# Performance work log

Measured on AMD Instinct MI355X. Metric: run time of the kernel, lower is better.

The kernel has to match this reference:

```python
import jax, jax.numpy as jnp
import numpy as np

B, N, C = 4, 1024, 768          # batch, tokens, embed_dim
D, H, HD, FF = 12, 12, 64, 3072  # depth, heads, head_dim, mlp hidden
LN_EPS = 1e-5


def setup_inputs() -> dict:
    key = jax.random.key(0)
    ks = jax.random.split(key, 12)
    w = lambda i, shape: jax.random.normal(ks[i], shape, jnp.float32) * 0.02
    return {
        "x": jax.random.normal(ks[0], (B, N, C), jnp.float32),
        "pos_x": jax.random.normal(ks[1], (B, N, C), jnp.float32),
        # stacked per-layer params (leading dim D)
        "qkv_w": w(2, (D, 3 * C, C)), "qkv_b": w(3, (D, 3 * C)),
        "proj_w": w(4, (D, C, C)),    "proj_b": w(5, (D, C)),
        "fc1_w": w(6, (D, FF, C)),    "fc1_b": w(7, (D, FF)),
        "fc2_w": w(8, (D, C, FF)),    "fc2_b": w(9, (D, C)),
        "ln1_g": jnp.ones((D, C), jnp.float32), "ln1_b": jnp.zeros((D, C), jnp.float32),
        "ln2_g": jnp.ones((D, C), jnp.float32), "ln2_b": jnp.zeros((D, C), jnp.float32),
        "normf_g": jnp.ones((C,), jnp.float32), "normf_b": jnp.zeros((C,), jnp.float32),
    }


def _ln(x, g, b):
    mu = jnp.mean(x, axis=-1, keepdims=True)
    var = jnp.mean((x - mu) ** 2, axis=-1, keepdims=True)
    return (x - mu) * jax.lax.rsqrt(var + LN_EPS) * g + b


def reference(x, pos_x, qkv_w, qkv_b, proj_w, proj_b, fc1_w, fc1_b, fc2_w, fc2_b,
              ln1_g, ln1_b, ln2_g, ln2_b, normf_g, normf_b):
    scale = 1.0 / jnp.sqrt(jnp.float32(HD))
    x = x + pos_x  # pos added once (add_pos_at_every_layer=False)

    def block(xc, p):
        qw, qb, pw, pb, f1w, f1b, f2w, f2b, g1, b1, g2, b2 = p
        h = _ln(xc, g1, b1)
        qkv = jnp.einsum('bnc,oc->bno', h, qw) + qb            # [B,N,3C]
        qkv = qkv.reshape(B, N, 3, H, HD).transpose(2, 0, 3, 1, 4)
        q, k, v = qkv[0], qkv[1], qkv[2]                       # [B,H,N,HD]
        attn = jax.nn.softmax(jnp.einsum('bhnd,bhmd->bhnm', q, k) * scale, axis=-1)
        o = jnp.einsum('bhnm,bhmd->bhnd', attn, v)
        o = o.transpose(0, 2, 1, 3).reshape(B, N, C)
        xc = xc + (jnp.einsum('bnc,oc->bno', o, pw) + pb)      # residual + proj
        h2 = _ln(xc, g2, b2)
        hid = jax.nn.gelu(jnp.einsum('bnc,fc->bnf', h2, f1w) + f1b, approximate=False)
        ffn = jnp.einsum('bnf,of->bno', hid, f2w) + f2b
        xc = xc + ffn
        return xc, None

    xs = (qkv_w, qkv_b, proj_w, proj_b, fc1_w, fc1_b, fc2_w, fc2_b,
          ln1_g, ln1_b, ln2_g, ln2_b)
    x, _ = jax.lax.scan(block, x, xs)
    return _ln(x, normf_g, normf_b)  # postnorm
```

## Files before the change

kernel.cpp:

```cpp
#include <hip/hip_runtime.h>
#include <hip/hip_bf16.h>
#include <math.h>

typedef __bf16 bf16;
typedef __bf16 bf16x8 __attribute__((ext_vector_type(8)));
typedef __bf16 bf16x4 __attribute__((ext_vector_type(4)));
typedef float  f32x4  __attribute__((ext_vector_type(4)));

#define B_  4
#define N_  1024
#define C_  768
#define H_  12
#define HD_ 64
#define FF_ 3072
#define T_  (B_*N_)
#define D_  12

__device__ __forceinline__ void gld_lds16(const void* g, void* l) {
    __builtin_amdgcn_global_load_lds(
        (const __attribute__((address_space(1))) void*)g,
        (__attribute__((address_space(3))) void*)l, 16, 0, 0);
}

template<typename WT, int MODE>
__global__ __launch_bounds__(256) void gemm_bt(
    const bf16* __restrict__ A, const WT* __restrict__ Bt,
    const float* __restrict__ bias, bf16* __restrict__ out,
    float* __restrict__ resid, int M, int N, int Kfull, int Ks)
{
    __shared__ __align__(16) bf16 lA[128*64];
    __shared__ __align__(16) WT   lB[128*64];
    const int tid  = threadIdx.x;
    const int lane = tid & 63, wave = tid >> 6;
    const int lo = lane & 15, hi = lane >> 4;
    const int wm = wave & 1, wn = wave >> 1;
    const int row0 = blockIdx.x * 128, col0 = blockIdx.y * 128;
    const int k0base = blockIdx.z * Ks;

    f32x4 acc[4][4];
#pragma unroll
    for (int i = 0; i < 4; i++)
#pragma unroll
        for (int j = 0; j < 4; j++) acc[i][j] = (f32x4){0.f, 0.f, 0.f, 0.f};

    for (int k0 = k0base; k0 < k0base + Ks; k0 += 64) {
#pragma unroll
        for (int r = 0; r < 4; ++r) {
            const int cb    = r * 256 + wave * 64;
            const int chunk = cb + lane;
            const int rw = chunk >> 3, kc = chunk & 7;
            const int kcs = kc ^ (rw & 7);
            gld_lds16(A + (size_t)(row0 + rw) * Kfull + k0 + kcs * 8, lA + cb * 8);
        }
        if constexpr (sizeof(WT) == 2) {
#pragma unroll
            for (int r = 0; r < 4; ++r) {
                const int cb    = r * 256 + wave * 64;
                const int chunk = cb + lane;
                const int rw = chunk >> 3, kc = chunk & 7;
                const int kcs = kc ^ (rw & 7);
                gld_lds16(Bt + (size_t)(col0 + rw) * Kfull + k0 + kcs * 8,
                          (bf16*)lB + cb * 8);
            }
        } else {
#pragma unroll
            for (int r = 0; r < 8; ++r) {
                const int cb    = r * 256 + wave * 64;
                const int chunk = cb + lane;
                const int rw = chunk >> 4, kc = chunk & 15;
                const int kcs = kc ^ ((rw & 7) << 1);
                gld_lds16(Bt + (size_t)(col0 + rw) * Kfull + k0 + kcs * 4,
                          (float*)lB + cb * 4);
            }
        }
        __syncthreads();
#pragma unroll 1
        for (int s = 0; s < 2; ++s) {
            bf16x8 af[4], bfr[4];
#pragma unroll
            for (int i = 0; i < 4; i++) {
                const int rowA = wm * 64 + i * 16 + lo;
                const int ca = (s * 4 + hi) ^ (lo & 7);
                af[i] = *(const bf16x8*)(lA + rowA * 64 + ca * 8);
            }
#pragma unroll
            for (int i = 0; i < 4; i++) {
                const int rowB = wn * 64 + i * 16 + lo;
                if constexpr (sizeof(WT) == 2) {
                    const int cb = (s * 4 + hi) ^ (lo & 7);
                    bfr[i] = *(const bf16x8*)((const bf16*)lB + rowB * 64 + cb * 8);
                } else {
                    const float* base = (const float*)lB + rowB * 64;
                    const int c0 = (s * 8 + hi * 2) ^ ((lo & 7) << 1);
                    const f32x4 u0 = *(const f32x4*)(base + c0 * 4);
                    const f32x4 u1 = *(const f32x4*)(base + (c0 + 1) * 4);
                    bf16x8 f;
#pragma unroll
                    for (int e = 0; e < 4; e++) { f[e] = (bf16)u0[e]; f[4+e] = (bf16)u1[e]; }
                    bfr[i] = f;
                }
            }
#pragma unroll
            for (int mi = 0; mi < 4; mi++)
#pragma unroll
                for (int ni = 0; ni < 4; ni++)
                    acc[mi][ni] = __builtin_amdgcn_mfma_f32_16x16x32_bf16(
                        af[mi], bfr[ni], acc[mi][ni], 0, 0, 0);
        }
        __syncthreads();
    }

    const float bscale = (blockIdx.z == 0) ? 1.0f : 0.0f;
#pragma unroll
    for (int mi = 0; mi < 4; mi++) {
#pragma unroll
        for (int ni = 0; ni < 4; ni++) {
            const int gcol = col0 + wn * 64 + ni * 16 + lo;
            const float bv = bias[gcol] * bscale;
#pragma unroll
            for (int r = 0; r < 4; r++) {
                const int grow = row0 + wm * 64 + mi * 16 + hi * 4 + r;
                float v = acc[mi][ni][r] + bv;
                if (MODE == 1) v = 0.5f * v * (1.0f + erff(v * 0.70710678118f));
                if (MODE == 2) {
                    atomicAdd(&resid[(size_t)grow * N + gcol], v);
                } else {
                    out[(size_t)grow * N + gcol] = (bf16)v;
                }
            }
        }
    }
}

__global__ __launch_bounds__(256) void cvt_k(
    const float* __restrict__ src, bf16* __restrict__ dst)
{
    const int i = (blockIdx.x * 256 + threadIdx.x) * 8;
    const f32x4 a = *(const f32x4*)(src + i);
    const f32x4 b = *(const f32x4*)(src + i + 4);
    bf16x8 o;
#pragma unroll
    for (int e = 0; e < 4; e++) { o[e] = (bf16)a[e]; o[4 + e] = (bf16)b[e]; }
    *(bf16x8*)(dst + i) = o;
}

template<typename OutT>
__global__ __launch_bounds__(256) void ln_k(
    const float* __restrict__ x, const float* __restrict__ g,
    const float* __restrict__ b, OutT* __restrict__ out)
{
    const int wave = threadIdx.x >> 6, lane = threadIdx.x & 63;
    const int t = blockIdx.x * 4 + wave;
    const float* row = x + (size_t)t * C_;
    f32x4 v[3];
    float s = 0.f, ss = 0.f;
#pragma unroll
    for (int j = 0; j < 3; j++) {
        v[j] = *(const f32x4*)(row + (j * 64 + lane) * 4);
#pragma unroll
        for (int e = 0; e < 4; e++) { s += v[j][e]; ss += v[j][e] * v[j][e]; }
    }
#pragma unroll
    for (int off = 32; off > 0; off >>= 1) {
        s  += __shfl_xor(s, off);
        ss += __shfl_xor(ss, off);
    }
    const float mu  = s * (1.f / 768.f);
    const float var = ss * (1.f / 768.f) - mu * mu;
    const float rs  = rsqrtf(var + 1e-5f);
    OutT* orow = out + (size_t)t * C_;
#pragma unroll
    for (int j = 0; j < 3; j++) {
        const f32x4 gv = *(const f32x4*)(g + (j * 64 + lane) * 4);
        const f32x4 bv = *(const f32x4*)(b + (j * 64 + lane) * 4);
#pragma unroll
        for (int e = 0; e < 4; e++)
            orow[(j * 64 + lane) * 4 + e] = (OutT)((v[j][e] - mu) * rs * gv[e] + bv[e]);
    }
}

__global__ __launch_bounds__(256) void addpos_k(
    const float* __restrict__ x, const float* __restrict__ p, float* __restrict__ o)
{
    const int i = (blockIdx.x * 256 + threadIdx.x) * 4;
    const f32x4 xv = *(const f32x4*)(x + i);
    const f32x4 pv = *(const f32x4*)(p + i);
    f32x4 ov;
#pragma unroll
    for (int e = 0; e < 4; e++) ov[e] = xv[e] + pv[e];
    *(f32x4*)(o + i) = ov;
}

#define SKD_ 72
#define SVK_ 136
#define SPK_ 136
__global__ __launch_bounds__(256) void attn_k(
    const bf16* __restrict__ qkv, bf16* __restrict__ out)
{
    const int qt = blockIdx.x;
    const int bh = blockIdx.y;
    const int b = bh / H_, h = bh % H_;
    const int lane = threadIdx.x & 63, wave = threadIdx.x >> 6;
    const int lo = lane & 15, hi = lane >> 4;

    __shared__ __align__(16) bf16 lK[128 * SKD_];
    __shared__ __align__(16) bf16 lV[64 * SVK_];
    __shared__ __align__(16) bf16 lP[4][16 * SPK_];

    const size_t tokbase = (size_t)b * N_;

    const bf16* qptr = qkv + (tokbase + qt * 64 + wave * 16 + lo) * (3 * C_) + h * HD_;
    bf16x8 qf0 = *(const bf16x8*)(qptr + hi * 8);
    bf16x8 qf1 = *(const bf16x8*)(qptr + 32 + hi * 8);
#pragma unroll
    for (int e = 0; e < 8; e++) {
        qf0[e] = (bf16)((float)qf0[e] * 0.125f);
        qf1[e] = (bf16)((float)qf1[e] * 0.125f);
    }

    float m_r[4], l_r[4];
    f32x4 oacc[4];
#pragma unroll
    for (int r = 0; r < 4; r++) { m_r[r] = -1e30f; l_r[r] = 0.f; }
#pragma unroll
    for (int di = 0; di < 4; di++) oacc[di] = (f32x4){0.f, 0.f, 0.f, 0.f};

    for (int kt = 0; kt < 8; ++kt) {
        const int kb0 = kt * 128;
#pragma unroll
        for (int r = 0; r < 4; ++r) {
            const int chunk = r * 256 + threadIdx.x;
            const int key = chunk >> 3, dc = chunk & 7;
            const bf16* kp = qkv + (tokbase + kb0 + key) * (3 * C_) + C_ + h * HD_ + dc * 8;
            *(bf16x8*)(lK + key * SKD_ + dc * 8) = *(const bf16x8*)kp;
        }
#pragma unroll
        for (int r = 0; r < 4; ++r) {
            const int chunk = r * 256 + threadIdx.x;
            const int d = chunk & 63, kg = chunk >> 6;
            const bf16* vp = qkv + (tokbase + kb0 + kg * 8) * (3 * C_)
                           + 2 * C_ + h * HD_ + d;
            bf16x8 tv;
#pragma unroll
            for (int i = 0; i < 8; i++) tv[i] = vp[(size_t)i * (3 * C_)];
            *(bf16x8*)(lV + d * SVK_ + kg * 8) = tv;
        }
        __syncthreads();

        f32x4 sacc[8];
#pragma unroll
        for (int kb = 0; kb < 8; kb++) {
            const bf16x8 b0 = *(const bf16x8*)(lK + (kb * 16 + lo) * SKD_ + hi * 8);
            const bf16x8 b1 = *(const bf16x8*)(lK + (kb * 16 + lo) * SKD_ + 32 + hi * 8);
            f32x4 a = (f32x4){0.f, 0.f, 0.f, 0.f};
            a = __builtin_amdgcn_mfma_f32_16x16x32_bf16(qf0, b0, a, 0, 0, 0);
            a = __builtin_amdgcn_mfma_f32_16x16x32_bf16(qf1, b1, a, 0, 0, 0);
            sacc[kb] = a;
        }

        float tm[4], mn[4], alpha[4], ts[4];
#pragma unroll
        for (int r = 0; r < 4; r++) {
            float a0 = fmaxf(fmaxf(sacc[0][r], sacc[1][r]),
                             fmaxf(sacc[2][r], sacc[3][r]));
            float a1 = fmaxf(fmaxf(sacc[4][r], sacc[5][r]),
                             fmaxf(sacc[6][r], sacc[7][r]));
            tm[r] = fmaxf(a0, a1);
#pragma unroll
            for (int off = 1; off < 16; off <<= 1)
                tm[r] = fmaxf(tm[r], __shfl_xor(tm[r], off));
            mn[r] = fmaxf(m_r[r], tm[r]);
            alpha[r] = __expf(m_r[r] - mn[r]);
            ts[r] = 0.f;
        }
#pragma unroll
        for (int kb = 0; kb < 8; kb++)
#pragma unroll
            for (int r = 0; r < 4; r++) {
                const float p = __expf(sacc[kb][r] - mn[r]);
                lP[wave][(hi * 4 + r) * SPK_ + kb * 16 + lo] = (bf16)p;
                ts[r] += p;
            }
#pragma unroll
        for (int r = 0; r < 4; r++) {
#pragma unroll
            for (int off = 1; off < 16; off <<= 1)
                ts[r] += __shfl_xor(ts[r], off);
            l_r[r] = l_r[r] * alpha[r] + ts[r];
            m_r[r] = mn[r];
        }
#pragma unroll
        for (int di = 0; di < 4; di++)
#pragma unroll
            for (int r = 0; r < 4; r++) oacc[di][r] *= alpha[r];

        bf16x8 pa[4];
#pragma unroll
        for (int s = 0; s < 4; s++)
            pa[s] = *(const bf16x8*)(&lP[wave][lo * SPK_ + s * 32 + hi * 8]);
#pragma unroll
        for (int di = 0; di < 4; di++) {
#pragma unroll
            for (int s = 0; s < 4; s++) {
                const bf16x8 v = *(const bf16x8*)(lV + (di * 16 + lo) * SVK_ + s * 32 + hi * 8);
                oacc[di] = __builtin_amdgcn_mfma_f32_16x16x32_bf16(pa[s], v, oacc[di], 0, 0, 0);
            }
        }
        __syncthreads();
    }

#pragma unroll
    for (int di = 0; di < 4; di++)
#pragma unroll
        for (int r = 0; r < 4; r++) {
            const size_t tok = tokbase + qt * 64 + wave * 16 + hi * 4 + r;
            out[tok * C_ + h * HD_ + di * 16 + lo] = (bf16)(oacc[di][r] / l_r[r]);
        }
}

extern "C" void kernel_launch(void* const* d_in, const int* in_sizes, int n_in,
                              void* d_out, int out_size, void* d_ws, size_t ws_size,
                              hipStream_t stream)
{
    const float* x      = (const float*)d_in[0];
    const float* pos_x  = (const float*)d_in[1];
    const float* qkv_w  = (const float*)d_in[2];
    const float* qkv_b  = (const float*)d_in[3];
    const float* proj_w = (const float*)d_in[4];
    const float* proj_b = (const float*)d_in[5];
    const float* fc1_w  = (const float*)d_in[6];
    const float* fc1_b  = (const float*)d_in[7];
    const float* fc2_w  = (const float*)d_in[8];
    const float* fc2_b  = (const float*)d_in[9];
    const float* ln1_g  = (const float*)d_in[10];
    const float* ln1_b  = (const float*)d_in[11];
    const float* ln2_g  = (const float*)d_in[12];
    const float* ln2_b  = (const float*)d_in[13];
    const float* nf_g   = (const float*)d_in[14];
    const float* nf_b   = (const float*)d_in[15];

    char* ws = (char*)d_ws;
    float* xres  = (float*)(ws);
    bf16* hbuf   = (bf16*)(ws + 12582912);
    bf16* qkvbuf = (bf16*)(ws + 18874368);
    bf16* attno  = (bf16*)(ws + 37748736);
    bf16* hid    = (bf16*)(ws + 44040192);
    bf16* wq     = (bf16*)(ws + 69206016);
    bf16* wp     = (bf16*)(ws + 111673344);
    bf16* w1     = (bf16*)(ws + 125829120);
    bf16* w2     = (bf16*)(ws + 182452224);
    const bool usebf16 = ws_size >= (size_t)239075328;

    addpos_k<<<T_ * C_ / 4 / 256, 256, 0, stream>>>(x, pos_x, xres);

    if (usebf16) {
        cvt_k<<<D_ * 3 * C_ * C_ / 2048, 256, 0, stream>>>(qkv_w, wq);
        cvt_k<<<D_ * C_ * C_ / 2048, 256, 0, stream>>>(proj_w, wp);
        cvt_k<<<D_ * FF_ * C_ / 2048, 256, 0, stream>>>(fc1_w, w1);
        cvt_k<<<D_ * C_ * FF_ / 2048, 256, 0, stream>>>(fc2_w, w2);
    }

    for (int L = 0; L < D_; ++L) {
        ln_k<bf16><<<T_ / 4, 256, 0, stream>>>(xres, ln1_g + L * C_, ln1_b + L * C_, hbuf);
        if (usebf16) {
            gemm_bt<bf16,0><<<dim3(T_/128, (3*C_)/128, 1), 256, 0, stream>>>(
                hbuf, wq + (size_t)L * 3 * C_ * C_, qkv_b + (size_t)L * 3 * C_,
                qkvbuf, nullptr, T_, 3 * C_, C_, C_);
        } else {
            gemm_bt<float,0><<<dim3(T_/128, (3*C_)/128, 1), 256, 0, stream>>>(
                hbuf, qkv_w + (size_t)L * 3 * C_ * C_, qkv_b + (size_t)L * 3 * C_,
                qkvbuf, nullptr, T_, 3 * C_, C_, C_);
        }
        attn_k<<<dim3(N_ / 64, B_ * H_), 256, 0, stream>>>(qkvbuf, attno);
        if (usebf16) {
            gemm_bt<bf16,2><<<dim3(T_/128, C_/128, 2), 256, 0, stream>>>(
                attno, wp + (size_t)L * C_ * C_, proj_b + (size_t)L * C_,
                nullptr, xres, T_, C_, C_, C_ / 2);
        } else {
            gemm_bt<float,2><<<dim3(T_/128, C_/128, 2), 256, 0, stream>>>(
                attno, proj_w + (size_t)L * C_ * C_, proj_b + (size_t)L * C_,
                nullptr, xres, T_, C_, C_, C_ / 2);
        }
        ln_k<bf16><<<T_ / 4, 256, 0, stream>>>(xres, ln2_g + L * C_, ln2_b + L * C_, hbuf);
        if (usebf16) {
            gemm_bt<bf16,1><<<dim3(T_/128, FF_/128, 1), 256, 0, stream>>>(
                hbuf, w1 + (size_t)L * FF_ * C_, fc1_b + (size_t)L * FF_,
                hid, nullptr, T_, FF_, C_, C_);
            gemm_bt<bf16,2><<<dim3(T_/128, C_/128, 2), 256, 0, stream>>>(
                hid, w2 + (size_t)L * C_ * FF_, fc2_b + (size_t)L * C_,
                nullptr, xres, T_, C_, FF_, FF_ / 2);
        } else {
            gemm_bt<float,1><<<dim3(T_/128, FF_/128, 1), 256, 0, stream>>>(
                hbuf, fc1_w + (size_t)L * FF_ * C_, fc1_b + (size_t)L * FF_,
                hid, nullptr, T_, FF_, C_, C_);
            gemm_bt<float,2><<<dim3(T_/128, C_/128, 2), 256, 0, stream>>>(
                hid, fc2_w + (size_t)L * C_ * FF_, fc2_b + (size_t)L * C_,
                nullptr, xres, T_, C_, FF_, FF_ / 2);
        }
    }
    ln_k<float><<<T_ / 4, 256, 0, stream>>>(xres, nf_g, nf_b, (float*)d_out);
}
```

Before: 2.647 ms.

## Remap GEMM and attention blocks across XCDs and defer softmax rescaling

```diff
diff --git a/kernel.cpp b/kernel.cpp
--- a/kernel.cpp
+++ b/kernel.cpp
@@ -34,8 +34,16 @@
     const int lane = tid & 63, wave = tid >> 6;
     const int lo = lane & 15, hi = lane >> 4;
     const int wm = wave & 1, wn = wave >> 1;
-    const int row0 = blockIdx.x * 128, col0 = blockIdx.y * 128;
-    const int k0base = blockIdx.z * Ks;
+
+    const int nblk = gridDim.x;
+    const int id2  = (blockIdx.x & 7) * (nblk >> 3) + (blockIdx.x >> 3);
+    const int gx = M >> 7, gy = N >> 7;
+    const int bx  = id2 % gx;
+    const int byz = id2 / gx;
+    const int by  = byz % gy;
+    const int bz  = byz / gy;
+    const int row0 = bx * 128, col0 = by * 128;
+    const int k0base = bz * Ks;
 
     f32x4 acc[4][4];
 #pragma unroll
@@ -110,7 +118,7 @@
         __syncthreads();
     }
 
-    const float bscale = (blockIdx.z == 0) ? 1.0f : 0.0f;
+    const float bscale = (bz == 0) ? 1.0f : 0.0f;
 #pragma unroll
     for (int mi = 0; mi < 4; mi++) {
 #pragma unroll
@@ -197,8 +205,9 @@
 __global__ __launch_bounds__(256) void attn_k(
     const bf16* __restrict__ qkv, bf16* __restrict__ out)
 {
-    const int qt = blockIdx.x;
-    const int bh = blockIdx.y;
+    const int id2 = (blockIdx.x & 7) * 96 + (blockIdx.x >> 3);
+    const int qt = id2 & 15;
+    const int bh = id2 >> 4;
     const int b = bh / H_, h = bh % H_;
     const int lane = threadIdx.x & 63, wave = threadIdx.x >> 6;
     const int lo = lane & 15, hi = lane >> 4;
@@ -258,20 +267,31 @@
             sacc[kb] = a;
         }
 
-        float tm[4], mn[4], alpha[4], ts[4];
+        float pm[4], mn[4], ts[4];
 #pragma unroll
         for (int r = 0; r < 4; r++) {
             float a0 = fmaxf(fmaxf(sacc[0][r], sacc[1][r]),
                              fmaxf(sacc[2][r], sacc[3][r]));
             float a1 = fmaxf(fmaxf(sacc[4][r], sacc[5][r]),
                              fmaxf(sacc[6][r], sacc[7][r]));
-            tm[r] = fmaxf(a0, a1);
-#pragma unroll
-            for (int off = 1; off < 16; off <<= 1)
-                tm[r] = fmaxf(tm[r], __shfl_xor(tm[r], off));
-            mn[r] = fmaxf(m_r[r], tm[r]);
-            alpha[r] = __expf(m_r[r] - mn[r]);
+            pm[r] = fmaxf(a0, a1);
             ts[r] = 0.f;
+        }
+        const int okd = (pm[0] <= m_r[0] + 8.f) && (pm[1] <= m_r[1] + 8.f)
+                     && (pm[2] <= m_r[2] + 8.f) && (pm[3] <= m_r[3] + 8.f);
+        const bool defer = __all(okd);
+        if (defer) {
+#pragma unroll
+            for (int r = 0; r < 4; r++) mn[r] = m_r[r];
+        } else {
+#pragma unroll
+            for (int r = 0; r < 4; r++) {
+                float tm = pm[r];
+#pragma unroll
+                for (int off = 1; off < 16; off <<= 1)
+                    tm = fmaxf(tm, __shfl_xor(tm, off));
+                mn[r] = fmaxf(m_r[r], tm);
+            }
         }
 #pragma unroll
         for (int kb = 0; kb < 8; kb++)
@@ -282,17 +302,26 @@
                 ts[r] += p;
             }
 #pragma unroll
-        for (int r = 0; r < 4; r++) {
+        for (int r = 0; r < 4; r++)
 #pragma unroll
             for (int off = 1; off < 16; off <<= 1)
                 ts[r] += __shfl_xor(ts[r], off);
-            l_r[r] = l_r[r] * alpha[r] + ts[r];
-            m_r[r] = mn[r];
-        }
-#pragma unroll
-        for (int di = 0; di < 4; di++)
-#pragma unroll
-            for (int r = 0; r < 4; r++) oacc[di][r] *= alpha[r];
+        if (defer) {
+#pragma unroll
+            for (int r = 0; r < 4; r++) l_r[r] += ts[r];
+        } else {
+            float alpha[4];
+#pragma unroll
+            for (int r = 0; r < 4; r++) {
+                alpha[r] = __expf(m_r[r] - mn[r]);
+                l_r[r] = l_r[r] * alpha[r] + ts[r];
+                m_r[r] = mn[r];
+            }
+#pragma unroll
+            for (int di = 0; di < 4; di++)
+#pragma unroll
+                for (int r = 0; r < 4; r++) oacc[di][r] *= alpha[r];
+        }
 
         bf16x8 pa[4];
 #pragma unroll
@@ -309,12 +338,15 @@
         __syncthreads();
     }
 
+    float il[4];
+#pragma unroll
+    for (int r = 0; r < 4; r++) il[r] = 1.0f / l_r[r];
 #pragma unroll
     for (int di = 0; di < 4; di++)
 #pragma unroll
         for (int r = 0; r < 4; r++) {
             const size_t tok = tokbase + qt * 64 + wave * 16 + hi * 4 + r;
-            out[tok * C_ + h * HD_ + di * 16 + lo] = (bf16)(oacc[di][r] / l_r[r]);
+            out[tok * C_ + h * HD_ + di * 16 + lo] = (bf16)(oacc[di][r] * il[r]);
         }
 }
 
@@ -360,40 +392,45 @@
         cvt_k<<<D_ * C_ * FF_ / 2048, 256, 0, stream>>>(fc2_w, w2);
     }
 
+    const int g_qkv  = (T_/128) * ((3*C_)/128);
+    const int g_proj = (T_/128) * (C_/128) * 2;
+    const int g_fc1  = (T_/128) * (FF_/128);
+    const int g_fc2  = (T_/128) * (C_/128) * 2;
+
     for (int L = 0; L < D_; ++L) {
         ln_k<bf16><<<T_ / 4, 256, 0, stream>>>(xres, ln1_g + L * C_, ln1_b + L * C_, hbuf);
         if (usebf16) {
-            gemm_bt<bf16,0><<<dim3(T_/128, (3*C_)/128, 1), 256, 0, stream>>>(
+            gemm_bt<bf16,0><<<g_qkv, 256, 0, stream>>>(
                 hbuf, wq + (size_t)L * 3 * C_ * C_, qkv_b + (size_t)L * 3 * C_,
                 qkvbuf, nullptr, T_, 3 * C_, C_, C_);
         } else {
-            gemm_bt<float,0><<<dim3(T_/128, (3*C_)/128, 1), 256, 0, stream>>>(
+            gemm_bt<float,0><<<g_qkv, 256, 0, stream>>>(
                 hbuf, qkv_w + (size_t)L * 3 * C_ * C_, qkv_b + (size_t)L * 3 * C_,
                 qkvbuf, nullptr, T_, 3 * C_, C_, C_);
         }
-        attn_k<<<dim3(N_ / 64, B_ * H_), 256, 0, stream>>>(qkvbuf, attno);
+        attn_k<<<N_ / 64 * B_ * H_, 256, 0, stream>>>(qkvbuf, attno);
         if (usebf16) {
-            gemm_bt<bf16,2><<<dim3(T_/128, C_/128, 2), 256, 0, stream>>>(
+            gemm_bt<bf16,2><<<g_proj, 256, 0, stream>>>(
                 attno, wp + (size_t)L * C_ * C_, proj_b + (size_t)L * C_,
                 nullptr, xres, T_, C_, C_, C_ / 2);
         } else {
-            gemm_bt<float,2><<<dim3(T_/128, C_/128, 2), 256, 0, stream>>>(
+            gemm_bt<float,2><<<g_proj, 256, 0, stream>>>(
                 attno, proj_w + (size_t)L * C_ * C_, proj_b + (size_t)L * C_,
                 nullptr, xres, T_, C_, C_, C_ / 2);
         }
         ln_k<bf16><<<T_ / 4, 256, 0, stream>>>(xres, ln2_g + L * C_, ln2_b + L * C_, hbuf);
         if (usebf16) {
-            gemm_bt<bf16,1><<<dim3(T_/128, FF_/128, 1), 256, 0, stream>>>(
+            gemm_bt<bf16,1><<<g_fc1, 256, 0, stream>>>(
                 hbuf, w1 + (size_t)L * FF_ * C_, fc1_b + (size_t)L * FF_,
                 hid, nullptr, T_, FF_, C_, C_);
-            gemm_bt<bf16,2><<<dim3(T_/128, C_/128, 2), 256, 0, stream>>>(
+            gemm_bt<bf16,2><<<g_fc2, 256, 0, stream>>>(
                 hid, w2 + (size_t)L * C_ * FF_, fc2_b + (size_t)L * C_,
                 nullptr, xres, T_, C_, FF_, FF_ / 2);
         } else {
-            gemm_bt<float,1><<<dim3(T_/128, FF_/128, 1), 256, 0, stream>>>(
+            gemm_bt<float,1><<<g_fc1, 256, 0, stream>>>(
                 hbuf, fc1_w + (size_t)L * FF_ * C_, fc1_b + (size_t)L * FF_,
                 hid, nullptr, T_, FF_, C_, C_);
-            gemm_bt<float,2><<<dim3(T_/128, C_/128, 2), 256, 0, stream>>>(
+            gemm_bt<float,2><<<g_fc2, 256, 0, stream>>>(
                 hid, fc2_w + (size_t)L * C_ * FF_, fc2_b + (size_t)L * C_,
                 nullptr, xres, T_, C_, FF_, FF_ / 2);
         }
```

After: 2.557 ms. -3.4%, faster.
